# Optimization experiments

Hardware: AMD Instinct MI355X
Metric: run time of the kernel (lower is better)

## Reference

```python
import jax, jax.numpy as jnp
import numpy as np

N, E, B = 150000, 600000, 1024
F_IN, F_HID = 78, 312          # 78 * 2**output_dim_power_0(=2)
OUT_DIM = 128
L, VOCAB, EMB = 1000, 26, 128  # num_features_xt+1 = 26 embedding rows
NF, KS = 8, 8                  # 2**n_filters_power, 2**kernel_size_power
CONV_FLAT = NF * (EMB - KS + 1)  # 8*121 = 968
K_HOPS = 2
SLOPE = 0.01                   # torch leaky_relu default

def _lin(k, i, o):
    s = 1.0 / np.sqrt(i)
    kw, kb = jax.random.split(k)
    return (jax.random.uniform(kw, (i, o), jnp.float32, -s, s),
            jax.random.uniform(kb, (o,), jnp.float32, -s, s))

def setup_inputs() -> dict:
    key = jax.random.key(0)
    ks = jax.random.split(key, 12)
    x = jax.random.normal(ks[0], (N, F_IN), jnp.float32)
    edge_index = jax.random.randint(ks[1], (2, E), 0, N)
    batch = (jnp.arange(N) * B) // N            # sorted graph ids, all B graphs nonempty
    target = jax.random.randint(ks[2], (B, L), 0, VOCAB)
    sgc_w, sgc_b = _lin(ks[3], F_IN, F_HID)
    fcg1_w, fcg1_b = _lin(ks[4], F_HID, OUT_DIM)
    emb_table = jax.random.normal(ks[5], (VOCAB, EMB), jnp.float32)
    sc = 1.0 / np.sqrt(L * KS)
    conv_w = jax.random.uniform(ks[6], (NF, L, KS), jnp.float32, -sc, sc)  # OIW
    conv_b = jax.random.uniform(ks[7], (NF,), jnp.float32, -sc, sc)
    fcxt_w, fcxt_b = _lin(ks[8], CONV_FLAT, OUT_DIM)
    fc1_w, fc1_b = _lin(ks[9], 2 * OUT_DIM, 1024)
    fc2_w, fc2_b = _lin(ks[10], 1024, 512)
    out_w, out_b = _lin(ks[11], 512, 1)
    return dict(x=x, sgc_w=sgc_w, sgc_b=sgc_b, fcg1_w=fcg1_w, fcg1_b=fcg1_b,
                emb_table=emb_table, conv_w=conv_w, conv_b=conv_b,
                fcxt_w=fcxt_w, fcxt_b=fcxt_b, fc1_w=fc1_w, fc1_b=fc1_b,
                fc2_w=fc2_w, fc2_b=fc2_b, out_w=out_w, out_b=out_b,
                edge_index=edge_index, batch=batch, target=target)

def reference(x, sgc_w, sgc_b, fcg1_w, fcg1_b, emb_table, conv_w, conv_b,
              fcxt_w, fcxt_b, fc1_w, fc1_b, fc2_w, fc2_b, out_w, out_b,
              edge_index, batch, target):
    # --- SGConv: K-hop symmetric-normalized propagation with self-loops, then linear ---
    loop = jnp.arange(N)
    src = jnp.concatenate([edge_index[0], loop])
    dst = jnp.concatenate([edge_index[1], loop])
    deg = jax.ops.segment_sum(jnp.ones_like(src, jnp.float32), dst, num_segments=N)
    dinv = jnp.where(deg > 0, jax.lax.rsqrt(deg), 0.0)
    norm = (dinv[src] * dinv[dst])[:, None]
    h = x
    for _ in range(K_HOPS):
        h = jax.ops.segment_sum(h[src] * norm, dst, num_segments=N)  # [N, F]
    h = jax.nn.leaky_relu(h @ sgc_w + sgc_b, SLOPE)                  # [N, 312]
    # --- global max pool per graph + fc_g1 ---
    g = jax.ops.segment_max(h, batch, num_segments=B)                # [B, 312]
    g = jax.nn.leaky_relu(g @ fcg1_w + fcg1_b, SLOPE)                # [B, 128]
    # --- protein branch: embed -> Conv1d(in=1000) over embed axis -> flatten -> fc ---
    emb = emb_table[target]                                          # [B, 1000, 128]
    conv = jax.lax.conv_general_dilated(emb, conv_w, (1,), 'VALID',
                                        dimension_numbers=('NCW', 'OIW', 'NCW'))
    conv = conv + conv_b[None, :, None]                              # [B, 8, 121]
    xt = conv.reshape(B, CONV_FLAT) @ fcxt_w + fcxt_b                # [B, 128]
    # --- head ---
    xc = jnp.concatenate([g, xt], axis=1)                            # [B, 256]
    xc = jax.nn.relu(xc @ fc1_w + fc1_b)
    xc = jax.nn.relu(xc @ fc2_w + fc2_b)
    return xc @ out_w + out_b                                        # [B, 1]
```

## Files before the change

kernel.cpp:

```cpp
#include <hip/hip_runtime.h>

#define N_NODES 150000
#define N_EDGES 600000
#define BATCH   1024
#define F_IN    78
#define HB_S    80
#define F_HID   312
#define OUT_DIMW 128
#define SEQ_L   1000
#define VOCAB   26
#define EMB     128
#define NF      8
#define KS      8
#define CONV_WO 121
#define CONV_FLAT 968
#define SK      208
#define SLOPE   0.01f
#define KEY_NEGMAX ((int)0x80800000)
#define SCAN_NBLK ((N_NODES + 255) / 256)

#define NT   20
#define BSW_HALF (3 * NT * 64 * 8)
#define M_PAD 150016
#define GM_BLKS (M_PAD / 128 * 2)
#define GM_CHUNK (GM_BLKS / 8)

#define WSW_HALF 65536

typedef __attribute__((ext_vector_type(8))) short bf8;
typedef __attribute__((ext_vector_type(4))) float f4;

__device__ __forceinline__ short f2bf(float f) {
  unsigned u = __float_as_uint(f);
  return (short)((u + 0x7fffu + ((u >> 16) & 1u)) >> 16);
}
__device__ __forceinline__ float bf2f(short h) {
  return __uint_as_float(((unsigned)(unsigned short)h) << 16);
}

__device__ __forceinline__ int fkey(float v) {
  int i = __float_as_int(v);
  return i >= 0 ? i : (i ^ 0x7fffffff);
}
__device__ __forceinline__ float fdec(int k) {
  return __int_as_float(k >= 0 ? k : (k ^ 0x7fffffff));
}

__global__ void k_zero_i(int* __restrict__ p, int n) {
  int i = blockIdx.x * blockDim.x + threadIdx.x;
  if (i < n) p[i] = 0;
}

__global__ void k_deg(const int* __restrict__ dst, int* __restrict__ deg) {
  int e = blockIdx.x * blockDim.x + threadIdx.x;
  if (e < N_EDGES) atomicAdd(&deg[dst[e]], 1);
}

__global__ __launch_bounds__(256) void k_scan1(const int* __restrict__ deg, int* __restrict__ rowptr,
                                               int* __restrict__ bsum, float* __restrict__ dinv) {
  __shared__ int s[256];
  int tid = threadIdx.x;
  int i = blockIdx.x * 256 + tid;
  int v = (i < N_NODES) ? deg[i] : 0;
  s[tid] = v;
  __syncthreads();
  int x = v;
  for (int o = 1; o < 256; o <<= 1) {
    int t = (tid >= o) ? s[tid - o] : 0;
    __syncthreads();
    x += t; s[tid] = x;
    __syncthreads();
  }
  if (i < N_NODES) {
    rowptr[i] = x - v;
    dinv[i] = rsqrtf((float)(v + 1));
  }
  if (tid == 255) bsum[blockIdx.x] = x;
}

__global__ __launch_bounds__(1024) void k_scan2(int* __restrict__ bsum) {
  __shared__ int s[1024];
  int tid = threadIdx.x;
  int v = (tid < SCAN_NBLK) ? bsum[tid] : 0;
  s[tid] = v;
  __syncthreads();
  int x = v;
  for (int o = 1; o < 1024; o <<= 1) {
    int t = (tid >= o) ? s[tid - o] : 0;
    __syncthreads();
    x += t; s[tid] = x;
    __syncthreads();
  }
  if (tid < SCAN_NBLK) bsum[tid] = x - v;
}

__global__ __launch_bounds__(256) void k_scan3(int* __restrict__ rowptr, const int* __restrict__ bsum,
                                               int* __restrict__ cnt) {
  int i = blockIdx.x * 256 + threadIdx.x;
  if (i < N_NODES) { rowptr[i] += bsum[blockIdx.x]; cnt[i] = 0; }
  if (i == 0) rowptr[N_NODES] = N_EDGES;
}

__global__ void k_fillcsr(const int* __restrict__ src, const int* __restrict__ dst,
                          const int* __restrict__ rowptr, int* __restrict__ cnt,
                          int* __restrict__ csr) {
  int e = blockIdx.x * blockDim.x + threadIdx.x;
  if (e < N_EDGES) {
    int d = dst[e];
    int pos = rowptr[d] + atomicAdd(&cnt[d], 1);
    csr[pos] = src[e];
  }
}

template<int HOP1>
__global__ __launch_bounds__(256) void k_pull(const int* __restrict__ rowptr,
                        const int* __restrict__ csr, const float* __restrict__ dinv,
                        const float* __restrict__ p, void* __restrict__ outv) {
  const int RS = HOP1 ? F_IN : HB_S;
  int dv = (int)((blockIdx.x * 256 + threadIdx.x) >> 6);
  if (dv >= N_NODES) return;
  int d = __builtin_amdgcn_readfirstlane(dv);
  int lane = threadIdx.x & 63;
  int j0 = rowptr[d], j1 = rowptr[d + 1];
  bool act = lane < 39;
  float dd = dinv[d];
  float2 aA = make_float2(0.f, 0.f), aB = aA, aC = aA, aD = aA;
  if (act) {
    float2 v = ((const float2*)(p + (size_t)d * RS))[lane];
    float c0 = HOP1 ? dd : 1.f;
    aA.x = c0 * v.x; aA.y = c0 * v.y;
  }
  int j = j0;
  for (; j + 3 < j1; j += 4) {
    int s0 = csr[j], s1 = csr[j + 1], s2 = csr[j + 2], s3 = csr[j + 3];
    float c0 = HOP1 ? dinv[s0] : 1.f, c1 = HOP1 ? dinv[s1] : 1.f;
    float c2 = HOP1 ? dinv[s2] : 1.f, c3 = HOP1 ? dinv[s3] : 1.f;
    if (act) {
      float2 u0 = ((const float2*)(p + (size_t)s0 * RS))[lane];
      float2 u1 = ((const float2*)(p + (size_t)s1 * RS))[lane];
      float2 u2 = ((const float2*)(p + (size_t)s2 * RS))[lane];
      float2 u3 = ((const float2*)(p + (size_t)s3 * RS))[lane];
      aA.x += c0 * u0.x; aA.y += c0 * u0.y;
      aB.x += c1 * u1.x; aB.y += c1 * u1.y;
      aC.x += c2 * u2.x; aC.y += c2 * u2.y;
      aD.x += c3 * u3.x; aD.y += c3 * u3.y;
    }
  }
  if (j + 1 < j1) {
    int s0 = csr[j], s1 = csr[j + 1];
    float c0 = HOP1 ? dinv[s0] : 1.f, c1 = HOP1 ? dinv[s1] : 1.f;
    if (act) {
      float2 u0 = ((const float2*)(p + (size_t)s0 * RS))[lane];
      float2 u1 = ((const float2*)(p + (size_t)s1 * RS))[lane];
      aA.x += c0 * u0.x; aA.y += c0 * u0.y;
      aB.x += c1 * u1.x; aB.y += c1 * u1.y;
    }
    j += 2;
  }
  if (j < j1) {
    int s0 = csr[j];
    float c0 = HOP1 ? dinv[s0] : 1.f;
    if (act) {
      float2 u0 = ((const float2*)(p + (size_t)s0 * RS))[lane];
      aC.x += c0 * u0.x; aC.y += c0 * u0.y;
    }
  }
  if (HOP1) {
    if (act) {
      float cs = dd * dd;
      ((float2*)((float*)outv + (size_t)d * HB_S))[lane] =
          make_float2(cs * (aA.x + aB.x + aC.x + aD.x), cs * (aA.y + aB.y + aC.y + aD.y));
    }
  } else {
    if (lane < 48) {
      float vx = dd * (aA.x + aB.x + aC.x + aD.x);
      float vy = dd * (aA.y + aB.y + aC.y + aD.y);
      short hx = f2bf(vx); short lx = f2bf(vx - bf2f(hx));
      short hy = f2bf(vy); short ly = f2bf(vy - bf2f(hy));
      int t = d >> 4, mrow = d & 15;
      int ksi = lane >> 4;
      int quad = (lane & 15) >> 2;
      int jj = (2 * lane) & 7;
      size_t base = (((size_t)(t * 3 + ksi) * 2) * 64 + quad * 16 + mrow) * 8 + jj;
      short* o = (short*)outv;
      *(unsigned*)(o + base) =
          (unsigned)(unsigned short)hx | ((unsigned)(unsigned short)hy << 16);
      *(unsigned*)(o + base + 512) =
          (unsigned)(unsigned short)lx | ((unsigned)(unsigned short)ly << 16);
    }
  }
}

template<int DEC>
__global__ __launch_bounds__(256) void k_gemm_sk(const float* __restrict__ A, const float* __restrict__ B,
                        float* __restrict__ Cp, int M, int N, int K, int kc) {
  __shared__ float As[16][33];
  __shared__ float Bs[16][68];
  int bm = blockIdx.x * 32, bn = blockIdx.y * 64;
  int k0s = blockIdx.z * kc;
  int k1s = min(K, k0s + kc);
  int tid = threadIdx.x;
  int tx = tid & 15, ty = tid >> 4;
  float acc[2][4] = {};
  for (int k0 = k0s; k0 < k1s; k0 += 16) {
    {
      int i2 = tid * 2;
      int m = i2 >> 4, k = i2 & 15;
      float2 av = make_float2(0.f, 0.f);
      const float* Ap = A + (size_t)(bm + m) * K + k0 + k;
      if (k0 + k + 1 < k1s)      av = *(const float2*)Ap;
      else if (k0 + k < k1s)     av.x = Ap[0];
      if (DEC) { av.x = fdec(__float_as_int(av.x)); av.y = fdec(__float_as_int(av.y)); }
      As[k][m] = av.x; As[k + 1][m] = av.y;
    }
    {
      int i4 = tid * 4;
      int kr = i4 >> 6, n = i4 & 63;
      float4 bv = make_float4(0.f, 0.f, 0.f, 0.f);
      if (k0 + kr < k1s) bv = *(const float4*)(B + (size_t)(k0 + kr) * N + bn + n);
      *(float4*)&Bs[kr][n] = bv;
    }
    __syncthreads();
#pragma unroll
    for (int kk = 0; kk < 16; kk++) {
      float a0 = As[kk][ty * 2], a1 = As[kk][ty * 2 + 1];
      float4 b = *(const float4*)&Bs[kk][tx * 4];
      acc[0][0] += a0 * b.x; acc[0][1] += a0 * b.y; acc[0][2] += a0 * b.z; acc[0][3] += a0 * b.w;
      acc[1][0] += a1 * b.x; acc[1][1] += a1 * b.y; acc[1][2] += a1 * b.z; acc[1][3] += a1 * b.w;
    }
    __syncthreads();
  }
#pragma unroll
  for (int im = 0; im < 2; im++) {
    int m = bm + ty * 2 + im;
    float4 v = make_float4(acc[im][0], acc[im][1], acc[im][2], acc[im][3]);
    *(float4*)(Cp + ((size_t)blockIdx.z * M + m) * N + bn + tx * 4) = v;
  }
}

template<int ACT>
__global__ __launch_bounds__(256) void k_gemm_dw(const float* __restrict__ A, const float* __restrict__ B,
                        const float* __restrict__ bias, float* __restrict__ C, int M, int N, int K) {
  __shared__ float As[16][33];
  __shared__ float Bs[16][68];
  int bm = blockIdx.x * 32, bn = blockIdx.y * 64;
  int tid = threadIdx.x;
  int tx = tid & 15, ty = tid >> 4;
  float acc[2][4] = {};
  for (int k0 = 0; k0 < K; k0 += 16) {
    {
      int i2 = tid * 2;
      int m = i2 >> 4, k = i2 & 15;
      float2 av = make_float2(0.f, 0.f);
      const float* Ap = A + (size_t)(bm + m) * K + k0 + k;
      if (k0 + k + 1 < K)      av = *(const float2*)Ap;
      else if (k0 + k < K)     av.x = Ap[0];
      As[k][m] = av.x; As[k + 1][m] = av.y;
    }
    {
      int i4 = tid * 4;
      int kr = i4 >> 6, n = i4 & 63;
      float4 bv = make_float4(0.f, 0.f, 0.f, 0.f);
      if (k0 + kr < K) bv = *(const float4*)(B + (size_t)(k0 + kr) * N + bn + n);
      *(float4*)&Bs[kr][n] = bv;
    }
    __syncthreads();
#pragma unroll
    for (int kk = 0; kk < 16; kk++) {
      float a0 = As[kk][ty * 2], a1 = As[kk][ty * 2 + 1];
      float4 b = *(const float4*)&Bs[kk][tx * 4];
      acc[0][0] += a0 * b.x; acc[0][1] += a0 * b.y; acc[0][2] += a0 * b.z; acc[0][3] += a0 * b.w;
      acc[1][0] += a1 * b.x; acc[1][1] += a1 * b.y; acc[1][2] += a1 * b.z; acc[1][3] += a1 * b.w;
    }
    __syncthreads();
  }
  float4 bv = *(const float4*)&bias[bn + tx * 4];
#pragma unroll
  for (int im = 0; im < 2; im++) {
    int m = bm + ty * 2 + im;
    float4 v = make_float4(acc[im][0] + bv.x, acc[im][1] + bv.y, acc[im][2] + bv.z, acc[im][3] + bv.w);
    if (ACT == 1) { v.x = fmaxf(v.x, 0.f); v.y = fmaxf(v.y, 0.f); v.z = fmaxf(v.z, 0.f); v.w = fmaxf(v.w, 0.f); }
    if (ACT == 2) { v.x = v.x > 0.f ? v.x : SLOPE * v.x; v.y = v.y > 0.f ? v.y : SLOPE * v.y;
                    v.z = v.z > 0.f ? v.z : SLOPE * v.z; v.w = v.w > 0.f ? v.w : SLOPE * v.w; }
    *(float4*)(C + (size_t)m * N + bn + tx * 4) = v;
  }
}

template<int ACT>
__global__ void k_sumact(const float* __restrict__ Cp, int S, const float* __restrict__ bias,
                         float* __restrict__ C, int nshift, int ldc, int coff) {
  int i = blockIdx.x * 256 + threadIdx.x;
  int MN = gridDim.x * 256;
  int m = i >> nshift, n = i & ((1 << nshift) - 1);
  float s = 0.f;
  for (int t = 0; t < S; t++) s += Cp[(size_t)t * MN + i];
  s += bias[n];
  if (ACT == 1) s = fmaxf(s, 0.f);
  if (ACT == 2) s = s > 0.f ? s : SLOPE * s;
  C[(size_t)m * ldc + coff + n] = s;
}

__global__ void k_prep(const float* __restrict__ B, short* __restrict__ Bsw,
                       const float* __restrict__ conv_w, short* __restrict__ Wsw,
                       int* __restrict__ gkeys) {
  int i = blockIdx.x * 256 + threadIdx.x;
  if (i < BATCH * F_HID) gkeys[i] = KEY_NEGMAX;
  if (i < BSW_HALF) {
    int j = i & 7;
    int lane = (i >> 3) & 63;
    int rest = i >> 9;
    int nt = rest % NT, ksi = rest / NT;
    int n = nt * 16 + (lane & 15);
    int k = ksi * 32 + (lane >> 4) * 8 + j;
    float v = (k < F_IN && n < F_HID) ? B[k * F_HID + n] : 0.f;
    short h = f2bf(v);
    Bsw[i] = h;
    Bsw[BSW_HALF + i] = f2bf(v - bf2f(h));
  }
  if (i < WSW_HALF) {
    int j = i & 7;
    int lane = (i >> 3) & 63;
    int rest = i >> 9;
    int nt = rest & 3, ks = rest >> 2;
    int fk = nt * 16 + (lane & 15);
    int l = ks * 32 + (lane >> 4) * 8 + j;
    float v = (l < SEQ_L) ? conv_w[(fk >> 3) * (SEQ_L * KS) + l * KS + (fk & 7)] : 0.f;
    short h = f2bf(v);
    Wsw[i] = h;
    Wsw[WSW_HALF + i] = f2bf(v - bf2f(h));
  }
}

__global__ __launch_bounds__(512) void k_gemm_max(const short* __restrict__ hA,
                           const short* __restrict__ Bsw,
                           const float* __restrict__ bias, int* __restrict__ gkeys) {
  __shared__ int red[2 * F_HID];
  int tid = threadIdx.x;

  int bid = blockIdx.x;
  int swz = (bid & 7) * GM_CHUNK + (bid >> 3);
  int mIdx = swz >> 1, nh2 = swz & 1;
  int m0 = mIdx * 128;

  int w = tid >> 6, lane = tid & 63;
  int mq = w & 3, nh = w >> 2;
  int ntb = (nh2 * 2 + nh) * 5;
  int mrow = lane & 15, quad = lane >> 4;

  int t0 = (m0 + mq * 32) >> 4;
  const short* apb = hA + (size_t)t0 * 3072 + (size_t)lane * 8;
  bf8 ah[2][3], al[2][3];
#pragma unroll
  for (int mi = 0; mi < 2; mi++)
#pragma unroll
    for (int ksi = 0; ksi < 3; ksi++) {
      const short* ap = apb + (size_t)(mi * 3 + ksi) * 1024;
      ah[mi][ksi] = *(const bf8*)ap;
      al[mi][ksi] = *(const bf8*)(ap + 512);
    }

  for (int i = tid; i < 2 * F_HID; i += 512) red[i] = KEY_NEGMAX;
  __syncthreads();

  f4 acc[2][5];
#pragma unroll
  for (int mi = 0; mi < 2; mi++)
#pragma unroll
    for (int j = 0; j < 5; j++) acc[mi][j] = (f4)0.f;

  const short* bbase = Bsw + ((size_t)ntb * 64 + lane) * 8;

#pragma unroll
  for (int ksi = 0; ksi < 3; ksi++) {
    const short* bh = bbase + (size_t)ksi * (NT * 512);
    const short* bl = bh + BSW_HALF;
#pragma unroll
    for (int j = 0; j < 5; j++) {
      bf8 bhv = *(const bf8*)(bh + j * 512);
      bf8 blv = *(const bf8*)(bl + j * 512);
#pragma unroll
      for (int mi = 0; mi < 2; mi++) {
        acc[mi][j] = __builtin_amdgcn_mfma_f32_16x16x32_bf16(ah[mi][ksi], bhv, acc[mi][j], 0, 0, 0);
        acc[mi][j] = __builtin_amdgcn_mfma_f32_16x16x32_bf16(al[mi][ksi], bhv, acc[mi][j], 0, 0, 0);
        acc[mi][j] = __builtin_amdgcn_mfma_f32_16x16x32_bf16(ah[mi][ksi], blv, acc[mi][j], 0, 0, 0);
      }
    }
  }

  int g0 = (int)(((long long)m0 * BATCH) / N_NODES);
#pragma unroll
  for (int mi = 0; mi < 2; mi++) {
    int mgrp = m0 + mq * 32 + mi * 16;
    int gg  = (int)(((long long)mgrp * BATCH) / N_NODES);
    int bndg = (int)((((long long)(gg + 1)) * N_NODES + BATCH - 1) / BATCH);
    int s = gg - g0;
    int mb = mgrp + quad * 4;
    if (bndg >= mgrp + 16 && mgrp + 16 <= N_NODES) {
#pragma unroll
      for (int j = 0; j < 5; j++) {
        int n = (ntb + j) * 16 + mrow;
        bool nok = n < F_HID;
        float bn = nok ? bias[n] : 0.f;
        float v0 = acc[mi][j][0] + bn; v0 = v0 > 0.f ? v0 : SLOPE * v0;
        float v1 = acc[mi][j][1] + bn; v1 = v1 > 0.f ? v1 : SLOPE * v1;
        float v2 = acc[mi][j][2] + bn; v2 = v2 > 0.f ? v2 : SLOPE * v2;
        float v3 = acc[mi][j][3] + bn; v3 = v3 > 0.f ? v3 : SLOPE * v3;
        float mx = fmaxf(fmaxf(v0, v1), fmaxf(v2, v3));
        mx = fmaxf(mx, __shfl_xor(mx, 16, 64));
        mx = fmaxf(mx, __shfl_xor(mx, 32, 64));
        if (quad == 0 && nok) atomicMax(&red[s * F_HID + n], fkey(mx));
      }
    } else {
#pragma unroll
      for (int j = 0; j < 5; j++) {
        int n = (ntb + j) * 16 + mrow;
        bool nok = n < F_HID;
        float bn = nok ? bias[n] : 0.f;
        float mx0 = -3.4e38f, mx1 = -3.4e38f;
#pragma unroll
        for (int r = 0; r < 4; r++) {
          int m = mb + r;
          if (m >= N_NODES) continue;
          float v = acc[mi][j][r] + bn;
          v = v > 0.f ? v : SLOPE * v;
          if (m >= bndg) mx1 = fmaxf(mx1, v); else mx0 = fmaxf(mx0, v);
        }
        mx0 = fmaxf(mx0, __shfl_xor(mx0, 16, 64));
        mx0 = fmaxf(mx0, __shfl_xor(mx0, 32, 64));
        mx1 = fmaxf(mx1, __shfl_xor(mx1, 16, 64));
        mx1 = fmaxf(mx1, __shfl_xor(mx1, 32, 64));
        if (quad == 0 && nok) {
          if (mx0 > -3.3e38f) atomicMax(&red[s * F_HID + n], fkey(mx0));
          if (mx1 > -3.3e38f && s == 0) atomicMax(&red[F_HID + n], fkey(mx1));
        }
      }
    }
  }
  __syncthreads();
  for (int i = tid; i < 2 * F_HID; i += 512) {
    int flag = i / F_HID, n = i - flag * F_HID;
    int g = g0 + flag;
    int key = red[i];
    if (g < BATCH && key != KEY_NEGMAX)
      atomicMax(&gkeys[g * F_HID + n], key);
  }
}

__global__ __launch_bounds__(256) void k_sbuild(const int* __restrict__ target,
                        const short* __restrict__ Wsw, float* __restrict__ Sg) {
  __shared__ int tl[4][1024];
  int tid = threadIdx.x;
  int w = tid >> 6, lane = tid & 63;
  int b = blockIdx.x * 4 + w;

  const int4* tg4 = (const int4*)(target + (size_t)b * SEQ_L);
  int4* tl4 = (int4*)&tl[w][0];
  for (int i = lane; i < 250; i += 64) tl4[i] = tg4[i];
  if (lane < 24) tl[w][1000 + lane] = -1;
  __syncthreads();

  int mrow = lane & 15, quad = lane >> 4;
  f4 acc[2][4];
#pragma unroll
  for (int mt = 0; mt < 2; mt++)
#pragma unroll
    for (int nt = 0; nt < 4; nt++) acc[mt][nt] = (f4)0.f;

  const short one = (short)0x3F80;
#pragma unroll 4
  for (int ks = 0; ks < 32; ks++) {
    int l0 = ks * 32 + quad * 8;
    int4 t0 = *(const int4*)&tl[w][l0];
    int4 t1 = *(const int4*)&tl[w][l0 + 4];
    int tv[8] = {t0.x, t0.y, t0.z, t0.w, t1.x, t1.y, t1.z, t1.w};
    bf8 a0, a1;
#pragma unroll
    for (int j = 0; j < 8; j++) {
      a0[j] = (tv[j] == mrow) ? one : (short)0;
      a1[j] = (tv[j] == mrow + 16) ? one : (short)0;
    }
    const short* bp = Wsw + ((size_t)(ks * 4) * 64 + lane) * 8;
    bf8 bh[4], bl[4];
#pragma unroll
    for (int nt = 0; nt < 4; nt++) {
      bh[nt] = *(const bf8*)(bp + nt * 512);
      bl[nt] = *(const bf8*)(bp + nt * 512 + WSW_HALF);
    }
#pragma unroll
    for (int nt = 0; nt < 4; nt++) {
      acc[0][nt] = __builtin_amdgcn_mfma_f32_16x16x32_bf16(a0, bh[nt], acc[0][nt], 0, 0, 0);
      acc[1][nt] = __builtin_amdgcn_mfma_f32_16x16x32_bf16(a1, bh[nt], acc[1][nt], 0, 0, 0);
    }
#pragma unroll
    for (int nt = 0; nt < 4; nt++) {
      acc[0][nt] = __builtin_amdgcn_mfma_f32_16x16x32_bf16(a0, bl[nt], acc[0][nt], 0, 0, 0);
      acc[1][nt] = __builtin_amdgcn_mfma_f32_16x16x32_bf16(a1, bl[nt], acc[1][nt], 0, 0, 0);
    }
  }

#pragma unroll
  for (int mt = 0; mt < 2; mt++)
#pragma unroll
    for (int nt = 0; nt < 4; nt++) {
      int fk = nt * 16 + mrow;
      float* sp = Sg + ((size_t)b * NF + (fk >> 3)) * SK + (fk & 7);
#pragma unroll
      for (int r = 0; r < 4; r++) {
        int v = mt * 16 + quad * 4 + r;
        if (v < VOCAB) sp[v * KS] = acc[mt][nt][r];
      }
    }
}

__global__ __launch_bounds__(256) void k_conv(const float* __restrict__ Sg, const float* __restrict__ emb,
                       const float* __restrict__ conv_b, float* __restrict__ convo) {
  __shared__ float Asub[32][SK];
  __shared__ float Etab[VOCAB * EMB];
  int r0 = blockIdx.x * 32;
  int tid = threadIdx.x;
  float* Af = &Asub[0][0];
  for (int i = tid; i < VOCAB * EMB; i += 256) Etab[i] = emb[i];
  for (int i = tid; i < 32 * SK; i += 256) Af[i] = Sg[(size_t)r0 * SK + i];
  __syncthreads();
  int w = tid & 127;
  int rg = tid >> 7;
  if (w < CONV_WO) {
    float acc[16] = {};
    for (int vk4 = 0; vk4 < SK; vk4 += 4) {
      int v0 = vk4 >> 3, k0 = vk4 & 7;
      float e0 = Etab[v0 * EMB + w + k0];
      float e1 = Etab[v0 * EMB + w + k0 + 1];
      float e2 = Etab[v0 * EMB + w + k0 + 2];
      float e3 = Etab[v0 * EMB + w + k0 + 3];
#pragma unroll
      for (int r = 0; r < 16; r++) {
        float4 a4 = *(const float4*)&Asub[rg * 16 + r][vk4];
        acc[r] += a4.x * e0 + a4.y * e1 + a4.z * e2 + a4.w * e3;
      }
    }
#pragma unroll
    for (int r = 0; r < 16; r++) {
      int row = r0 + rg * 16 + r;
      convo[(size_t)row * CONV_WO + w] = acc[r] + conv_b[row & 7];
    }
  }
}

__global__ void k_out(const float* __restrict__ a2, const float* __restrict__ w,
                      const float* __restrict__ b, float* __restrict__ out) {
  int row = (blockIdx.x * blockDim.x + threadIdx.x) >> 6;
  int lane = threadIdx.x & 63;
  if (row >= BATCH) return;
  const float* ar = a2 + (size_t)row * 512;
  float s = 0.f;
  for (int j = lane; j < 512; j += 64) s += ar[j] * w[j];
  for (int o = 32; o > 0; o >>= 1) s += __shfl_down(s, o, 64);
  if (lane == 0) out[row] = s + b[0];
}

extern "C" void kernel_launch(void* const* d_in, const int* in_sizes, int n_in,
                              void* d_out, int out_size, void* d_ws, size_t ws_size,
                              hipStream_t stream) {
  const float* x      = (const float*)d_in[0];
  const float* sgc_w  = (const float*)d_in[1];
  const float* sgc_b  = (const float*)d_in[2];
  const float* fcg1_w = (const float*)d_in[3];
  const float* fcg1_b = (const float*)d_in[4];
  const float* emb    = (const float*)d_in[5];
  const float* conv_w = (const float*)d_in[6];
  const float* conv_b = (const float*)d_in[7];
  const float* fcxt_w = (const float*)d_in[8];
  const float* fcxt_b = (const float*)d_in[9];
  const float* fc1_w  = (const float*)d_in[10];
  const float* fc1_b  = (const float*)d_in[11];
  const float* fc2_w  = (const float*)d_in[12];
  const float* fc2_b  = (const float*)d_in[13];
  const float* out_w  = (const float*)d_in[14];
  const float* out_b  = (const float*)d_in[15];
  const int* edge     = (const int*)d_in[16];
  const int* target   = (const int*)d_in[18];
  float* out = (float*)d_out;

  char* ws = (char*)d_ws;
  size_t off = 0;
  auto take = [&](size_t bytes) {
    void* p = ws + off;
    off += (bytes + 255) & ~(size_t)255;
    return p;
  };
  int*      deg    = (int*)     take((size_t)N_NODES * 4);
  float*    dinv   = (float*)   take((size_t)N_NODES * 4);
  int*      rowptr = (int*)     take((size_t)(N_NODES + 1) * 4);
  int*      bsum   = (int*)     take((size_t)SCAN_NBLK * 4);
  int*      cnt    = (int*)     take((size_t)N_NODES * 4);
  int*      csr    = (int*)     take((size_t)N_EDGES * 4);
  short*    hA     = (short*)   take((size_t)M_PAD * 192 * 2);
  float*    hB     = (float*)   take((size_t)N_NODES * HB_S * 4);
  short*    Bsw    = (short*)   take((size_t)2 * BSW_HALF * 2);
  short*    Wsw    = (short*)   take((size_t)2 * WSW_HALF * 2);
  int*      gkeys  = (int*)     take((size_t)BATCH * F_HID * 4);
  float*    Sg     = (float*)   take((size_t)BATCH * NF * SK * 4);
  float*    convo  = (float*)   take((size_t)BATCH * NF * CONV_WO * 4);
  float*    xc     = (float*)   take((size_t)BATCH * 256 * 4);
  float*    a1     = (float*)   take((size_t)BATCH * 1024 * 4);
  float*    a2     = (float*)   take((size_t)BATCH * 512 * 4);
  float*    psum   = hB;

  const int* esrc = edge;
  const int* edst = edge + N_EDGES;

  k_zero_i<<<(N_NODES + 255) / 256, 256, 0, stream>>>(deg, N_NODES);
  k_deg<<<(N_EDGES + 255) / 256, 256, 0, stream>>>(edst, deg);
  k_scan1<<<SCAN_NBLK, 256, 0, stream>>>(deg, rowptr, bsum, dinv);
  k_scan2<<<1, 1024, 0, stream>>>(bsum);
  k_scan3<<<SCAN_NBLK, 256, 0, stream>>>(rowptr, bsum, cnt);
  k_fillcsr<<<(N_EDGES + 255) / 256, 256, 0, stream>>>(esrc, edst, rowptr, cnt, csr);

  k_prep<<<(BATCH * F_HID + 255) / 256, 256, 0, stream>>>(sgc_w, Bsw, conv_w, Wsw, gkeys);

  k_pull<1><<<(N_NODES * 64 + 255) / 256, 256, 0, stream>>>(rowptr, csr, dinv, x, hB);
  k_pull<0><<<(N_NODES * 64 + 255) / 256, 256, 0, stream>>>(rowptr, csr, dinv, hB, hA);

  k_gemm_max<<<GM_BLKS, 512, 0, stream>>>(hA, Bsw, sgc_b, gkeys);

  {
    dim3 g(BATCH / 32, OUT_DIMW / 64, 4);
    k_gemm_sk<1><<<g, 256, 0, stream>>>((const float*)gkeys, fcg1_w, psum, BATCH, OUT_DIMW, F_HID, 80);
    k_sumact<2><<<(BATCH * OUT_DIMW) / 256, 256, 0, stream>>>(psum, 4, fcg1_b, xc, 7, 256, 0);
  }

  k_sbuild<<<BATCH / 4, 256, 0, stream>>>(target, Wsw, Sg);
  k_conv<<<(BATCH * NF) / 32, 256, 0, stream>>>(Sg, emb, conv_b, convo);
  {
    dim3 g(BATCH / 32, OUT_DIMW / 64, 8);
    k_gemm_sk<0><<<g, 256, 0, stream>>>(convo, fcxt_w, psum, BATCH, OUT_DIMW, CONV_FLAT, 128);
    k_sumact<0><<<(BATCH * OUT_DIMW) / 256, 256, 0, stream>>>(psum, 8, fcxt_b, xc, 7, 256, OUT_DIMW);
  }

  {
    dim3 g(BATCH / 32, 1024 / 64);
    k_gemm_dw<1><<<g, 256, 0, stream>>>(xc, fc1_w, fc1_b, a1, BATCH, 1024, 256);
  }
  {
    dim3 g(BATCH / 32, 512 / 64, 4);
    k_gemm_sk<0><<<g, 256, 0, stream>>>(a1, fc2_w, psum, BATCH, 512, 1024, 256);
    k_sumact<1><<<(BATCH * 512) / 256, 256, 0, stream>>>(psum, 4, fc2_b, a2, 9, 512, 0);
  }
  k_out<<<(BATCH * 64) / 256, 256, 0, stream>>>(a2, out_w, out_b, out);
}
```

Before: 482.6 us.

## Fuse CSR build into cooperative kernel, merge sbuild+conv, drop split-K GEMMs

Merges the zero, degree, three scan stages, CSR fill and prep kernels into one cooperative kernel separated by grid-wide syncs. It also fuses the S-build and conv kernels so the intermediate stays in shared memory instead of global memory. The split-K GEMMs and their reduction kernels are replaced with direct GEMMs that apply bias and activation in place. The goal is fewer launches and less intermediate traffic, at the cost of grid syncs, a serial block-sum scan, and less parallelism in the small GEMMs (fc2 now gets only 256 blocks).

After: 916.8 us. 1.9x slower.

```diff
diff --git a/kernel.cpp b/kernel.cpp
--- a/kernel.cpp
+++ b/kernel.cpp
@@ -1,4 +1,7 @@
 #include <hip/hip_runtime.h>
+#include <hip/hip_cooperative_groups.h>
+
+namespace cg = cooperative_groups;
 
 #define N_NODES 150000
 #define N_EDGES 600000
@@ -46,69 +49,86 @@
   return __int_as_float(k >= 0 ? k : (k ^ 0x7fffffff));
 }
 
-__global__ void k_zero_i(int* __restrict__ p, int n) {
-  int i = blockIdx.x * blockDim.x + threadIdx.x;
-  if (i < n) p[i] = 0;
-}
-
-__global__ void k_deg(const int* __restrict__ dst, int* __restrict__ deg) {
-  int e = blockIdx.x * blockDim.x + threadIdx.x;
-  if (e < N_EDGES) atomicAdd(&deg[dst[e]], 1);
-}
-
-__global__ __launch_bounds__(256) void k_scan1(const int* __restrict__ deg, int* __restrict__ rowptr,
-                                               int* __restrict__ bsum, float* __restrict__ dinv) {
+__global__ __launch_bounds__(256) void k_build(const int* __restrict__ esrc, const int* __restrict__ edst,
+        int* __restrict__ deg, int* __restrict__ rowptr, int* __restrict__ bsum,
+        float* __restrict__ dinv, int* __restrict__ cnt, int* __restrict__ csr,
+        const float* __restrict__ sgc_w, short* __restrict__ Bsw,
+        const float* __restrict__ conv_w, short* __restrict__ Wsw, int* __restrict__ gkeys) {
+  cg::grid_group grid = cg::this_grid();
   __shared__ int s[256];
-  int tid = threadIdx.x;
-  int i = blockIdx.x * 256 + tid;
-  int v = (i < N_NODES) ? deg[i] : 0;
-  s[tid] = v;
-  __syncthreads();
-  int x = v;
-  for (int o = 1; o < 256; o <<= 1) {
-    int t = (tid >= o) ? s[tid - o] : 0;
+  __shared__ int sb[SCAN_NBLK];
+  int tid = threadIdx.x, bid = blockIdx.x;
+  int gid = bid * 256 + tid;
+  const int gsz = SCAN_NBLK * 256;
+
+  for (int i = gid; i < N_NODES; i += gsz) deg[i] = 0;
+  for (int i = gid; i < BATCH * F_HID; i += gsz) gkeys[i] = KEY_NEGMAX;
+  for (int i = gid; i < BSW_HALF; i += gsz) {
+    int j = i & 7; int lane = (i >> 3) & 63; int rest = i >> 9;
+    int nt = rest % NT, ksi = rest / NT;
+    int n = nt * 16 + (lane & 15);
+    int k = ksi * 32 + (lane >> 4) * 8 + j;
+    float v = (k < F_IN && n < F_HID) ? sgc_w[k * F_HID + n] : 0.f;
+    short h = f2bf(v);
+    Bsw[i] = h; Bsw[BSW_HALF + i] = f2bf(v - bf2f(h));
+  }
+  for (int i = gid; i < WSW_HALF; i += gsz) {
+    int j = i & 7; int lane = (i >> 3) & 63; int rest = i >> 9;
+    int nt = rest & 3, ks = rest >> 2;
+    int fk = nt * 16 + (lane & 15);
+    int l = ks * 32 + (lane >> 4) * 8 + j;
+    float v = (l < SEQ_L) ? conv_w[(fk >> 3) * (SEQ_L * KS) + l * KS + (fk & 7)] : 0.f;
+    short h = f2bf(v);
+    Wsw[i] = h; Wsw[WSW_HALF + i] = f2bf(v - bf2f(h));
+  }
+  grid.sync();
+
+  for (int e = gid; e < N_EDGES; e += gsz) atomicAdd(&deg[edst[e]], 1);
+  grid.sync();
+
+  {
+    int i = gid;
+    int v = (i < N_NODES) ? deg[i] : 0;
+    s[tid] = v;
     __syncthreads();
-    x += t; s[tid] = x;
+    int x = v;
+    for (int o = 1; o < 256; o <<= 1) {
+      int t = (tid >= o) ? s[tid - o] : 0;
+      __syncthreads();
+      x += t; s[tid] = x;
+      __syncthreads();
+    }
+    if (i < N_NODES) {
+      rowptr[i] = x - v;
+      dinv[i] = rsqrtf((float)(v + 1));
+    }
+    if (tid == 255) bsum[bid] = x;
+  }
+  grid.sync();
+
+  if (bid == 0) {
+    for (int i = tid; i < SCAN_NBLK; i += 256) sb[i] = bsum[i];
     __syncthreads();
-  }
-  if (i < N_NODES) {
-    rowptr[i] = x - v;
-    dinv[i] = rsqrtf((float)(v + 1));
-  }
-  if (tid == 255) bsum[blockIdx.x] = x;
-}
-
-__global__ __launch_bounds__(1024) void k_scan2(int* __restrict__ bsum) {
-  __shared__ int s[1024];
-  int tid = threadIdx.x;
-  int v = (tid < SCAN_NBLK) ? bsum[tid] : 0;
-  s[tid] = v;
-  __syncthreads();
-  int x = v;
-  for (int o = 1; o < 1024; o <<= 1) {
-    int t = (tid >= o) ? s[tid - o] : 0;
+    if (tid == 0) {
+      int run = 0;
+      for (int i = 0; i < SCAN_NBLK; i++) { int v = sb[i]; sb[i] = run; run += v; }
+    }
     __syncthreads();
-    x += t; s[tid] = x;
-    __syncthreads();
-  }
-  if (tid < SCAN_NBLK) bsum[tid] = x - v;
-}
-
-__global__ __launch_bounds__(256) void k_scan3(int* __restrict__ rowptr, const int* __restrict__ bsum,
-                                               int* __restrict__ cnt) {
-  int i = blockIdx.x * 256 + threadIdx.x;
-  if (i < N_NODES) { rowptr[i] += bsum[blockIdx.x]; cnt[i] = 0; }
-  if (i == 0) rowptr[N_NODES] = N_EDGES;
-}
-
-__global__ void k_fillcsr(const int* __restrict__ src, const int* __restrict__ dst,
-                          const int* __restrict__ rowptr, int* __restrict__ cnt,
-                          int* __restrict__ csr) {
-  int e = blockIdx.x * blockDim.x + threadIdx.x;
-  if (e < N_EDGES) {
-    int d = dst[e];
+    for (int i = tid; i < SCAN_NBLK; i += 256) bsum[i] = sb[i];
+  }
+  grid.sync();
+
+  {
+    int i = gid;
+    if (i < N_NODES) { rowptr[i] += bsum[bid]; cnt[i] = 0; }
+    if (i == 0) rowptr[N_NODES] = N_EDGES;
+  }
+  grid.sync();
+
+  for (int e = gid; e < N_EDGES; e += gsz) {
+    int d = edst[e];
     int pos = rowptr[d] + atomicAdd(&cnt[d], 1);
-    csr[pos] = src[e];
+    csr[pos] = esrc[e];
   }
 }
 
@@ -191,56 +211,10 @@
   }
 }
 
-template<int DEC>
-__global__ __launch_bounds__(256) void k_gemm_sk(const float* __restrict__ A, const float* __restrict__ B,
-                        float* __restrict__ Cp, int M, int N, int K, int kc) {
-  __shared__ float As[16][33];
-  __shared__ float Bs[16][68];
-  int bm = blockIdx.x * 32, bn = blockIdx.y * 64;
-  int k0s = blockIdx.z * kc;
-  int k1s = min(K, k0s + kc);
-  int tid = threadIdx.x;
-  int tx = tid & 15, ty = tid >> 4;
-  float acc[2][4] = {};
-  for (int k0 = k0s; k0 < k1s; k0 += 16) {
-    {
-      int i2 = tid * 2;
-      int m = i2 >> 4, k = i2 & 15;
-      float2 av = make_float2(0.f, 0.f);
-      const float* Ap = A + (size_t)(bm + m) * K + k0 + k;
-      if (k0 + k + 1 < k1s)      av = *(const float2*)Ap;
-      else if (k0 + k < k1s)     av.x = Ap[0];
-      if (DEC) { av.x = fdec(__float_as_int(av.x)); av.y = fdec(__float_as_int(av.y)); }
-      As[k][m] = av.x; As[k + 1][m] = av.y;
-    }
-    {
-      int i4 = tid * 4;
-      int kr = i4 >> 6, n = i4 & 63;
-      float4 bv = make_float4(0.f, 0.f, 0.f, 0.f);
-      if (k0 + kr < k1s) bv = *(const float4*)(B + (size_t)(k0 + kr) * N + bn + n);
-      *(float4*)&Bs[kr][n] = bv;
-    }
-    __syncthreads();
-#pragma unroll
-    for (int kk = 0; kk < 16; kk++) {
-      float a0 = As[kk][ty * 2], a1 = As[kk][ty * 2 + 1];
-      float4 b = *(const float4*)&Bs[kk][tx * 4];
-      acc[0][0] += a0 * b.x; acc[0][1] += a0 * b.y; acc[0][2] += a0 * b.z; acc[0][3] += a0 * b.w;
-      acc[1][0] += a1 * b.x; acc[1][1] += a1 * b.y; acc[1][2] += a1 * b.z; acc[1][3] += a1 * b.w;
-    }
-    __syncthreads();
-  }
-#pragma unroll
-  for (int im = 0; im < 2; im++) {
-    int m = bm + ty * 2 + im;
-    float4 v = make_float4(acc[im][0], acc[im][1], acc[im][2], acc[im][3]);
-    *(float4*)(Cp + ((size_t)blockIdx.z * M + m) * N + bn + tx * 4) = v;
-  }
-}
-
-template<int ACT>
+template<int ACT, int DEC>
 __global__ __launch_bounds__(256) void k_gemm_dw(const float* __restrict__ A, const float* __restrict__ B,
-                        const float* __restrict__ bias, float* __restrict__ C, int M, int N, int K) {
+                        const float* __restrict__ bias, float* __restrict__ C,
+                        int M, int N, int K, int ldc, int coff) {
   __shared__ float As[16][33];
   __shared__ float Bs[16][68];
   int bm = blockIdx.x * 32, bn = blockIdx.y * 64;
@@ -255,6 +229,7 @@
       const float* Ap = A + (size_t)(bm + m) * K + k0 + k;
       if (k0 + k + 1 < K)      av = *(const float2*)Ap;
       else if (k0 + k < K)     av.x = Ap[0];
+      if (DEC) { av.x = fdec(__float_as_int(av.x)); av.y = fdec(__float_as_int(av.y)); }
       As[k][m] = av.x; As[k + 1][m] = av.y;
     }
     {
@@ -282,52 +257,7 @@
     if (ACT == 1) { v.x = fmaxf(v.x, 0.f); v.y = fmaxf(v.y, 0.f); v.z = fmaxf(v.z, 0.f); v.w = fmaxf(v.w, 0.f); }
     if (ACT == 2) { v.x = v.x > 0.f ? v.x : SLOPE * v.x; v.y = v.y > 0.f ? v.y : SLOPE * v.y;
                     v.z = v.z > 0.f ? v.z : SLOPE * v.z; v.w = v.w > 0.f ? v.w : SLOPE * v.w; }
-    *(float4*)(C + (size_t)m * N + bn + tx * 4) = v;
-  }
-}
-
-template<int ACT>
-__global__ void k_sumact(const float* __restrict__ Cp, int S, const float* __restrict__ bias,
-                         float* __restrict__ C, int nshift, int ldc, int coff) {
-  int i = blockIdx.x * 256 + threadIdx.x;
-  int MN = gridDim.x * 256;
-  int m = i >> nshift, n = i & ((1 << nshift) - 1);
-  float s = 0.f;
-  for (int t = 0; t < S; t++) s += Cp[(size_t)t * MN + i];
-  s += bias[n];
-  if (ACT == 1) s = fmaxf(s, 0.f);
-  if (ACT == 2) s = s > 0.f ? s : SLOPE * s;
-  C[(size_t)m * ldc + coff + n] = s;
-}
-
-__global__ void k_prep(const float* __restrict__ B, short* __restrict__ Bsw,
-                       const float* __restrict__ conv_w, short* __restrict__ Wsw,
-                       int* __restrict__ gkeys) {
-  int i = blockIdx.x * 256 + threadIdx.x;
-  if (i < BATCH * F_HID) gkeys[i] = KEY_NEGMAX;
-  if (i < BSW_HALF) {
-    int j = i & 7;
-    int lane = (i >> 3) & 63;
-    int rest = i >> 9;
-    int nt = rest % NT, ksi = rest / NT;
-    int n = nt * 16 + (lane & 15);
-    int k = ksi * 32 + (lane >> 4) * 8 + j;
-    float v = (k < F_IN && n < F_HID) ? B[k * F_HID + n] : 0.f;
-    short h = f2bf(v);
-    Bsw[i] = h;
-    Bsw[BSW_HALF + i] = f2bf(v - bf2f(h));
-  }
-  if (i < WSW_HALF) {
-    int j = i & 7;
-    int lane = (i >> 3) & 63;
-    int rest = i >> 9;
-    int nt = rest & 3, ks = rest >> 2;
-    int fk = nt * 16 + (lane & 15);
-    int l = ks * 32 + (lane >> 4) * 8 + j;
-    float v = (l < SEQ_L) ? conv_w[(fk >> 3) * (SEQ_L * KS) + l * KS + (fk & 7)] : 0.f;
-    short h = f2bf(v);
-    Wsw[i] = h;
-    Wsw[WSW_HALF + i] = f2bf(v - bf2f(h));
+    *(float4*)(C + (size_t)m * ldc + coff + bn + tx * 4) = v;
   }
 }
 
@@ -446,13 +376,17 @@
   }
 }
 
-__global__ __launch_bounds__(256) void k_sbuild(const int* __restrict__ target,
-                        const short* __restrict__ Wsw, float* __restrict__ Sg) {
+__global__ __launch_bounds__(256) void k_sconv(const int* __restrict__ target,
+                        const short* __restrict__ Wsw, const float* __restrict__ emb,
+                        const float* __restrict__ conv_b, float* __restrict__ convo) {
   __shared__ int tl[4][1024];
+  __shared__ float Asub[32][SK];
+  __shared__ float Etab[VOCAB * EMB];
   int tid = threadIdx.x;
   int w = tid >> 6, lane = tid & 63;
   int b = blockIdx.x * 4 + w;
 
+  for (int i = tid; i < VOCAB * EMB; i += 256) Etab[i] = emb[i];
   const int4* tg4 = (const int4*)(target + (size_t)b * SEQ_L);
   int4* tl4 = (int4*)&tl[w][0];
   for (int i = lane; i < 250; i += 64) tl4[i] = tg4[i];
@@ -503,45 +437,35 @@
 #pragma unroll
     for (int nt = 0; nt < 4; nt++) {
       int fk = nt * 16 + mrow;
-      float* sp = Sg + ((size_t)b * NF + (fk >> 3)) * SK + (fk & 7);
+      int f = fk >> 3, k = fk & 7;
 #pragma unroll
       for (int r = 0; r < 4; r++) {
         int v = mt * 16 + quad * 4 + r;
-        if (v < VOCAB) sp[v * KS] = acc[mt][nt][r];
+        if (v < VOCAB) Asub[w * 8 + f][v * 8 + k] = acc[mt][nt][r];
       }
     }
-}
-
-__global__ __launch_bounds__(256) void k_conv(const float* __restrict__ Sg, const float* __restrict__ emb,
-                       const float* __restrict__ conv_b, float* __restrict__ convo) {
-  __shared__ float Asub[32][SK];
-  __shared__ float Etab[VOCAB * EMB];
-  int r0 = blockIdx.x * 32;
-  int tid = threadIdx.x;
-  float* Af = &Asub[0][0];
-  for (int i = tid; i < VOCAB * EMB; i += 256) Etab[i] = emb[i];
-  for (int i = tid; i < 32 * SK; i += 256) Af[i] = Sg[(size_t)r0 * SK + i];
   __syncthreads();
-  int w = tid & 127;
+
+  int ww = tid & 127;
   int rg = tid >> 7;
-  if (w < CONV_WO) {
-    float acc[16] = {};
+  if (ww < CONV_WO) {
+    float acc2[16] = {};
     for (int vk4 = 0; vk4 < SK; vk4 += 4) {
       int v0 = vk4 >> 3, k0 = vk4 & 7;
-      float e0 = Etab[v0 * EMB + w + k0];
-      float e1 = Etab[v0 * EMB + w + k0 + 1];
-      float e2 = Etab[v0 * EMB + w + k0 + 2];
-      float e3 = Etab[v0 * EMB + w + k0 + 3];
+      float e0 = Etab[v0 * EMB + ww + k0];
+      float e1 = Etab[v0 * EMB + ww + k0 + 1];
+      float e2 = Etab[v0 * EMB + ww + k0 + 2];
+      float e3 = Etab[v0 * EMB + ww + k0 + 3];
 #pragma unroll
       for (int r = 0; r < 16; r++) {
         float4 a4 = *(const float4*)&Asub[rg * 16 + r][vk4];
-        acc[r] += a4.x * e0 + a4.y * e1 + a4.z * e2 + a4.w * e3;
+        acc2[r] += a4.x * e0 + a4.y * e1 + a4.z * e2 + a4.w * e3;
       }
     }
 #pragma unroll
     for (int r = 0; r < 16; r++) {
-      int row = r0 + rg * 16 + r;
-      convo[(size_t)row * CONV_WO + w] = acc[r] + conv_b[row & 7];
+      int row = blockIdx.x * 32 + rg * 16 + r;
+      convo[(size_t)row * CONV_WO + ww] = acc2[r] + conv_b[row & 7];
     }
   }
 }
@@ -599,24 +523,20 @@
   short*    Bsw    = (short*)   take((size_t)2 * BSW_HALF * 2);
   short*    Wsw    = (short*)   take((size_t)2 * WSW_HALF * 2);
   int*      gkeys  = (int*)     take((size_t)BATCH * F_HID * 4);
-  float*    Sg     = (float*)   take((size_t)BATCH * NF * SK * 4);
   float*    convo  = (float*)   take((size_t)BATCH * NF * CONV_WO * 4);
   float*    xc     = (float*)   take((size_t)BATCH * 256 * 4);
   float*    a1     = (float*)   take((size_t)BATCH * 1024 * 4);
   float*    a2     = (float*)   take((size_t)BATCH * 512 * 4);
-  float*    psum   = hB;
 
   const int* esrc = edge;
   const int* edst = edge + N_EDGES;
 
-  k_zero_i<<<(N_NODES + 255) / 256, 256, 0, stream>>>(deg, N_NODES);
-  k_deg<<<(N_EDGES + 255) / 256, 256, 0, stream>>>(edst, deg);
-  k_scan1<<<SCAN_NBLK, 256, 0, stream>>>(deg, rowptr, bsum, dinv);
-  k_scan2<<<1, 1024, 0, stream>>>(bsum);
-  k_scan3<<<SCAN_NBLK, 256, 0, stream>>>(rowptr, bsum, cnt);
-  k_fillcsr<<<(N_EDGES + 255) / 256, 256, 0, stream>>>(esrc, edst, rowptr, cnt, csr);
-
-  k_prep<<<(BATCH * F_HID + 255) / 256, 256, 0, stream>>>(sgc_w, Bsw, conv_w, Wsw, gkeys);
+  {
+    void* args[] = { (void*)&esrc, (void*)&edst, (void*)&deg, (void*)&rowptr, (void*)&bsum,
+                     (void*)&dinv, (void*)&cnt, (void*)&csr, (void*)&sgc_w, (void*)&Bsw,
+                     (void*)&conv_w, (void*)&Wsw, (void*)&gkeys };
+    hipLaunchCooperativeKernel((void*)k_build, dim3(SCAN_NBLK), dim3(256), args, 0, stream);
+  }
 
   k_pull<1><<<(N_NODES * 64 + 255) / 256, 256, 0, stream>>>(rowptr, csr, dinv, x, hB);
   k_pull<0><<<(N_NODES * 64 + 255) / 256, 256, 0, stream>>>(rowptr, csr, dinv, hB, hA);
@@ -624,27 +544,26 @@
   k_gemm_max<<<GM_BLKS, 512, 0, stream>>>(hA, Bsw, sgc_b, gkeys);
 
   {
-    dim3 g(BATCH / 32, OUT_DIMW / 64, 4);
-    k_gemm_sk<1><<<g, 256, 0, stream>>>((const float*)gkeys, fcg1_w, psum, BATCH, OUT_DIMW, F_HID, 80);
-    k_sumact<2><<<(BATCH * OUT_DIMW) / 256, 256, 0, stream>>>(psum, 4, fcg1_b, xc, 7, 256, 0);
-  }
-
-  k_sbuild<<<BATCH / 4, 256, 0, stream>>>(target, Wsw, Sg);
-  k_conv<<<(BATCH * NF) / 32, 256, 0, stream>>>(Sg, emb, conv_b, convo);
-  {
-    dim3 g(BATCH / 32, OUT_DIMW / 64, 8);
-    k_gemm_sk<0><<<g, 256, 0, stream>>>(convo, fcxt_w, psum, BATCH, OUT_DIMW, CONV_FLAT, 128);
-    k_sumact<0><<<(BATCH * OUT_DIMW) / 256, 256, 0, stream>>>(psum, 8, fcxt_b, xc, 7, 256, OUT_DIMW);
+    dim3 g(BATCH / 32, OUT_DIMW / 64);
+    k_gemm_dw<2, 1><<<g, 256, 0, stream>>>((const float*)gkeys, fcg1_w, fcg1_b, xc,
+                                           BATCH, OUT_DIMW, F_HID, 256, 0);
+  }
+
+  k_sconv<<<BATCH / 4, 256, 0, stream>>>(target, Wsw, emb, conv_b, convo);
+
+  {
+    dim3 g(BATCH / 32, OUT_DIMW / 64);
+    k_gemm_dw<0, 0><<<g, 256, 0, stream>>>(convo, fcxt_w, fcxt_b, xc,
+                                           BATCH, OUT_DIMW, CONV_FLAT, 256, 128);
   }
 
   {
     dim3 g(BATCH / 32, 1024 / 64);
-    k_gemm_dw<1><<<g, 256, 0, stream>>>(xc, fc1_w, fc1_b, a1, BATCH, 1024, 256);
-  }
-  {
-    dim3 g(BATCH / 32, 512 / 64, 4);
-    k_gemm_sk<0><<<g, 256, 0, stream>>>(a1, fc2_w, psum, BATCH, 512, 1024, 256);
-    k_sumact<1><<<(BATCH * 512) / 256, 256, 0, stream>>>(psum, 4, fc2_b, a2, 9, 512, 0);
+    k_gemm_dw<1, 0><<<g, 256, 0, stream>>>(xc, fc1_w, fc1_b, a1, BATCH, 1024, 256, 1024, 0);
+  }
+  {
+    dim3 g(BATCH / 32, 512 / 64);
+    k_gemm_dw<1, 0><<<g, 256, 0, stream>>>(a1, fc2_w, fc2_b, a2, BATCH, 512, 1024, 512, 0);
   }
   k_out<<<(BATCH * 64) / 256, 256, 0, stream>>>(a2, out_w, out_b, out);
 }
```
